# Optimization experiments

Hardware: AMD Instinct MI355X
Metric: run time of the kernel (lower is better)

The kernel has to match this reference:

```python
import jax, jax.numpy as jnp
import numpy as np

EMB = 1024
HEADS = 16
HEAD_DIM = EMB // HEADS
EPS = 1e-5


def setup_inputs() -> dict:
    key = jax.random.key(0)
    ks = jax.random.split(key, 10)
    B, T, D = 2, 2048, EMB
    s = 1.0 / np.sqrt(D)
    inp = {
        "x": jax.random.normal(ks[0], (B, T, D), dtype=jnp.float32),
        "wq": jax.random.normal(ks[1], (D, D), dtype=jnp.float32) * s,
        "bq": jnp.zeros((D,), jnp.float32),
        "wk": jax.random.normal(ks[2], (D, D), dtype=jnp.float32) * s,
        "bk": jnp.zeros((D,), jnp.float32),
        "wv": jax.random.normal(ks[3], (D, D), dtype=jnp.float32) * s,
        "bv": jnp.zeros((D,), jnp.float32),
        "wo": jax.random.normal(ks[4], (D, D), dtype=jnp.float32) * s,
        "bo": jnp.zeros((D,), jnp.float32),
        "gamma": jnp.ones((D,), jnp.float32),
        "beta": jnp.zeros((D,), jnp.float32),
    }
    return inp


def _attention(x, wq, bq, wk, bk, wv, bv, wo, bo, gamma, beta):
    B, T, D = x.shape
    H, Hd = HEADS, HEAD_DIM
    q = (x @ wq + bq).reshape(B, T, H, Hd)
    k = (x @ wk + bk).reshape(B, T, H, Hd)
    v = (x @ wv + bv).reshape(B, T, H, Hd)
    # scores: [B, H, T, T]
    scores = jnp.einsum("bthd,bshd->bhts", q, k) / np.sqrt(Hd)
    attn = jax.nn.softmax(scores, axis=-1)  # dropout is identity in eval
    ctx = jnp.einsum("bhts,bshd->bthd", attn, v).reshape(B, T, D)
    out = ctx @ wo + bo
    y = x + out  # residual (dropout identity)
    mu = jnp.mean(y, axis=-1, keepdims=True)
    var = jnp.var(y, axis=-1, keepdims=True)
    return (y - mu) * jax.lax.rsqrt(var + EPS) * gamma + beta


def reference(x, wq, bq, wk, bk, wv, bv, wo, bo, gamma, beta):
    return _attention(x, wq, bq, wk, bk, wv, bv, wo, bo, gamma, beta)
```

## Files before the change

### kernel.cpp

```cpp
#include <hip/hip_runtime.h>

#define BSZ   2
#define TSEQ  2048
#define DMOD  1024
#define NHEAD 16
#define HDIM  64
#define MROW  (BSZ*TSEQ)
#define LNEPS 1e-5f
#define QSCALE 0.18033688011f

typedef __bf16 bf16x8 __attribute__((ext_vector_type(8)));
typedef float  f32x4  __attribute__((ext_vector_type(4)));
typedef unsigned short us8 __attribute__((ext_vector_type(8)));
typedef unsigned short us4 __attribute__((ext_vector_type(4)));

__device__ __forceinline__ unsigned short f2bf(float f) {
    unsigned u = __float_as_uint(f);
    u += 0x7FFF + ((u >> 16) & 1);
    return (unsigned short)(u >> 16);
}

__device__ __forceinline__ float fexp2(float x) {
#if __has_builtin(__builtin_amdgcn_exp2f)
    return __builtin_amdgcn_exp2f(x);
#else
    return __expf(x * 0.6931471805599453f);
#endif
}

__device__ __forceinline__ void gld_lds16(const void* g, void* l) {
    __builtin_amdgcn_global_load_lds(
        (const __attribute__((address_space(1))) unsigned int*)g,
        (__attribute__((address_space(3))) unsigned int*)l, 16, 0, 0);
}

__global__ __launch_bounds__(256) void cvtx_k(const float* __restrict__ x,
                                              unsigned short* __restrict__ Xb)
{
    const size_t i = ((size_t)blockIdx.x * 256 + threadIdx.x) * 8;
    float4 a = *(const float4*)&x[i];
    float4 b = *(const float4*)&x[i + 4];
    union { unsigned short u[8]; uint4 v; } o;
    o.u[0] = f2bf(a.x); o.u[1] = f2bf(a.y); o.u[2] = f2bf(a.z); o.u[3] = f2bf(a.w);
    o.u[4] = f2bf(b.x); o.u[5] = f2bf(b.y); o.u[6] = f2bf(b.z); o.u[7] = f2bf(b.w);
    *(uint4*)&Xb[i] = o.v;
}

__global__ __launch_bounds__(256) void wt_all_k(
    const float* __restrict__ wq, const float* __restrict__ wk,
    const float* __restrict__ wv, const float* __restrict__ wo,
    unsigned short* __restrict__ WqkvT, unsigned short* __restrict__ WoT)
{
    __shared__ float T[64][68];
    const int z = blockIdx.z;
    const float* W = (z == 0) ? wq : (z == 1) ? wk : (z == 2) ? wv : wo;
    unsigned short* Wt = (z < 3) ? (WqkvT + (size_t)z*1024*1024) : WoT;
    const int tid = threadIdx.x;
    const int bx = blockIdx.x, by = blockIdx.y;
    const int lr = tid >> 4, lc = (tid & 15) * 4;
    #pragma unroll
    for (int p = 0; p < 4; ++p) {
        const int kk = p*16 + lr;
        float4 v = *(const float4*)&W[(size_t)(by*64 + kk)*1024 + bx*64 + lc];
        T[lc+0][kk] = v.x; T[lc+1][kk] = v.y; T[lc+2][kk] = v.z; T[lc+3][kk] = v.w;
    }
    __syncthreads();
    #pragma unroll
    for (int p = 0; p < 2; ++p) {
        const int nl = p*32 + (tid >> 3);
        const int kb = (tid & 7) * 8;
        float4 a = *(const float4*)&T[nl][kb];
        float4 b = *(const float4*)&T[nl][kb+4];
        union { unsigned short u[8]; uint4 v; } o;
        o.u[0]=f2bf(a.x); o.u[1]=f2bf(a.y); o.u[2]=f2bf(a.z); o.u[3]=f2bf(a.w);
        o.u[4]=f2bf(b.x); o.u[5]=f2bf(b.y); o.u[6]=f2bf(b.z); o.u[7]=f2bf(b.w);
        *(uint4*)&Wt[(size_t)(bx*64 + nl)*1024 + by*64 + kb] = o.v;
    }
}

template<int MODE>
__global__ __launch_bounds__(256) void gemm_bf16_k(
    const unsigned short* __restrict__ A, const unsigned short* __restrict__ Bt,
    const float* __restrict__ b0, const float* __restrict__ b1,
    const float* __restrict__ b2,
    void* __restrict__ o0, void* __restrict__ o1, void* __restrict__ o2)
{
    __shared__ unsigned short As[128*32];
    __shared__ unsigned short Bs[128*32];
    const int tid  = threadIdx.x;
    const int wv   = tid >> 6;
    const int lane = tid & 63;
    const int quad = lane >> 4;
    const int l16  = lane & 15;
    const int wm   = wv & 1, wn = wv >> 1;
    const int bm = blockIdx.y * 128, bn = blockIdx.x * 128;

    const int r0 = lane >> 2;
    const int jb = lane & 3;
    const unsigned short* Ag[2]; const unsigned short* Bg[2];
    void *ldsA[2], *ldsB[2];
    #pragma unroll
    for (int j = 0; j < 2; ++j) {
        const int c = wv*2 + j;
        const int R = c*16 + r0;
        const int gb = (jb ^ ((R >> 1) & 3)) * 8;
        Ag[j] = A  + (size_t)(bm + R)*1024 + gb;
        Bg[j] = Bt + (size_t)(bn + R)*1024 + gb;
        ldsA[j] = (char*)As + c*1024;
        ldsB[j] = (char*)Bs + c*1024;
    }

    const int asw = (quad ^ ((l16 >> 1) & 3)) * 8;
    const unsigned short* ap[4]; const unsigned short* bp[4];
    #pragma unroll
    for (int t = 0; t < 4; ++t) {
        ap[t] = &As[(wm*64 + t*16 + l16)*32 + asw];
        bp[t] = &Bs[(wn*64 + t*16 + l16)*32 + asw];
    }

    f32x4 acc[4][4];
    #pragma unroll
    for (int i = 0; i < 4; ++i)
        #pragma unroll
        for (int j = 0; j < 4; ++j) acc[i][j] = (f32x4){0.f,0.f,0.f,0.f};

    for (int k0 = 0; k0 < 1024; k0 += 32) {
        __syncthreads();
        gld_lds16(Ag[0] + k0, ldsA[0]);
        gld_lds16(Ag[1] + k0, ldsA[1]);
        gld_lds16(Bg[0] + k0, ldsB[0]);
        gld_lds16(Bg[1] + k0, ldsB[1]);
        __syncthreads();
        bf16x8 af[4], bfr[4];
        #pragma unroll
        for (int t = 0; t < 4; ++t) {
            af[t]  = *(const bf16x8*)ap[t];
            bfr[t] = *(const bf16x8*)bp[t];
        }
        #pragma unroll
        for (int i = 0; i < 4; ++i)
            #pragma unroll
            for (int j = 0; j < 4; ++j)
                acc[i][j] = __builtin_amdgcn_mfma_f32_16x16x32_bf16(af[i], bfr[j], acc[i][j], 0, 0, 0);
    }

    if (MODE == 0) {
        float* C = (float*)o0;
        #pragma unroll
        for (int nt = 0; nt < 4; ++nt) {
            const int gcol = bn + wn*64 + nt*16 + l16;
            const float bs = b0[gcol];
            #pragma unroll
            for (int mt = 0; mt < 4; ++mt)
                #pragma unroll
                for (int r = 0; r < 4; ++r) {
                    const int grow = bm + wm*64 + mt*16 + quad*4 + r;
                    C[(size_t)grow*1024 + gcol] = acc[mt][nt][r] + bs;
                }
        }
    } else {
        const int seg = bn >> 10;
        const float* bias = (seg == 0) ? b0 : (seg == 1) ? b1 : b2;
        const int cb = bn & 1023;
        if (seg < 2) {
            unsigned short* O = (unsigned short*)((seg == 0) ? o0 : o1);
            const float sc = (seg == 0) ? QSCALE : 1.0f;
            #pragma unroll
            for (int nt = 0; nt < 4; ++nt) {
                const int col = cb + wn*64 + nt*16 + l16;
                const float bs = bias[col];
                #pragma unroll
                for (int mt = 0; mt < 4; ++mt)
                    #pragma unroll
                    for (int r = 0; r < 4; ++r) {
                        const int grow = bm + wm*64 + mt*16 + quad*4 + r;
                        O[(size_t)grow*1024 + col] = f2bf((acc[mt][nt][r] + bs) * sc);
                    }
            }
        } else {
            unsigned short* O = (unsigned short*)o2;
            #pragma unroll
            for (int nt = 0; nt < 4; ++nt) {
                const int ch = cb + wn*64 + nt*16 + l16;
                const float bs = bias[ch];
                #pragma unroll
                for (int mt = 0; mt < 4; ++mt) {
                    const int grow0 = bm + wm*64 + mt*16 + quad*4;
                    us4 o;
                    #pragma unroll
                    for (int r = 0; r < 4; ++r) o[r] = f2bf(acc[mt][nt][r] + bs);
                    *(us4*)&O[(size_t)ch*MROW + grow0] = o;
                }
            }
        }
    }
}

__global__ __launch_bounds__(256, 2) void attn_k(
    const unsigned short* __restrict__ Qg,
    const unsigned short* __restrict__ Kg,
    const unsigned short* __restrict__ Vtg,
    unsigned short* __restrict__ CTX)
{
    __shared__ __align__(16) char lds_raw[51200];
    unsigned short* Qs = (unsigned short*)lds_raw;
    unsigned short* Ks = (unsigned short*)(lds_raw + 18432);
    unsigned short* Vs = (unsigned short*)(lds_raw + 34816);
    float* Od = (float*)lds_raw;
    float* Ld = (float*)(lds_raw + 34816);

    const int tid  = threadIdx.x;
    const int wv   = tid >> 6;
    const int lane = tid & 63;
    const int quad = lane >> 4;
    const int l16  = lane & 15;
    const int wq   = wv & 1;
    const int wk   = wv >> 1;
    const int qb   = blockIdx.x * 128;
    const int h    = blockIdx.y;
    const int b    = blockIdx.z;

    {
        const int row = tid & 127, cb = (tid >> 7) * 32;
        const unsigned short* Qrow = Qg + ((size_t)(b*TSEQ + qb + row))*DMOD + h*HDIM + cb;
        #pragma unroll
        for (int j = 0; j < 4; ++j)
            *(us8*)&Qs[row*72 + cb + j*8] = *(const us8*)&Qrow[j*8];
    }
    __syncthreads();
    bf16x8 qf[4][2];
    #pragma unroll
    for (int nt = 0; nt < 4; ++nt)
        #pragma unroll
        for (int kh = 0; kh < 2; ++kh)
            qf[nt][kh] = *(const bf16x8*)&Qs[(wq*64 + nt*16 + l16)*72 + kh*32 + quad*8];

    const int sr = lane >> 3;
    const int sc = lane & 7;
    const bool isK = (wv < 2);
    const int half = wv & 1;
    const unsigned short* gbase;
    unsigned int goff[8];
    unsigned short* ldst;
    if (isK) {
        gbase = Kg + ((size_t)(b*TSEQ + half*1024))*DMOD + h*HDIM;
        #pragma unroll
        for (int s = 0; s < 8; ++s) {
            const int R = s*8 + sr;
            const int gc = sc ^ ((R ^ (R >> 2)) & 7);
            goff[s] = (unsigned)(R*DMOD + gc*8);
        }
        ldst = Ks + half*4096;
    } else {
        gbase = Vtg + ((size_t)(h*HDIM))*MROW + b*TSEQ + half*1024;
        #pragma unroll
        for (int s = 0; s < 8; ++s) {
            const int D = s*8 + sr;
            const int gc = sc ^ (D & 7);
            goff[s] = (unsigned)(D*MROW + gc*8);
        }
        ldst = Vs + half*4096;
    }
    const size_t gstep = isK ? (size_t)64*DMOD : (size_t)64;

    const int rowA_l = (l16 >> 2)*8 + (l16 & 3);
    const int rowB_l = rowA_l + 4;
    const int swA = (rowA_l ^ (rowA_l >> 2)) & 7;
    const int swB = (rowB_l ^ (rowB_l >> 2)) & 7;
    const unsigned short* KsW = Ks + wk*4096;
    const unsigned short* VsW = Vs + wk*4096;

    bf16x8 onef;
    { union { unsigned short u[8]; bf16x8 v; } o1;
      #pragma unroll
      for (int i = 0; i < 8; ++i) o1.u[i] = 0x3F80;
      onef = o1.v; }

    f32x4 oacc[4][4];
    f32x4 lacc[4];
    #pragma unroll
    for (int dt = 0; dt < 4; ++dt)
        #pragma unroll
        for (int nt = 0; nt < 4; ++nt) oacc[dt][nt] = (f32x4){0.f,0.f,0.f,0.f};
    #pragma unroll
    for (int nt = 0; nt < 4; ++nt) lacc[nt] = (f32x4){0.f,0.f,0.f,0.f};

    for (int it = 0; it < 16; ++it) {
        __syncthreads();
        #pragma unroll
        for (int s = 0; s < 8; ++s)
            gld_lds16(gbase + (size_t)it*gstep + goff[s], ldst + s*512);
        __syncthreads();

        #pragma unroll
        for (int gl = 0; gl < 2; ++gl) {
            const int rA = gl*32 + rowA_l;
            const int rB = gl*32 + rowB_l;
            bf16x8 ka0 = *(const bf16x8*)&KsW[rA*64 + ((quad     ^ swA))*8];
            bf16x8 ka1 = *(const bf16x8*)&KsW[rA*64 + (((4+quad) ^ swA))*8];
            bf16x8 kb0 = *(const bf16x8*)&KsW[rB*64 + ((quad     ^ swB))*8];
            bf16x8 kb1 = *(const bf16x8*)&KsW[rB*64 + (((4+quad) ^ swB))*8];
            bf16x8 vf[4];
            #pragma unroll
            for (int dt = 0; dt < 4; ++dt)
                vf[dt] = *(const bf16x8*)&VsW[(dt*16 + l16)*64 + ((gl*4 + quad) ^ (l16 & 7))*8];

            #pragma unroll
            for (int nt = 0; nt < 4; ++nt) {
                f32x4 z = (f32x4){0.f,0.f,0.f,0.f};
                z = __builtin_amdgcn_mfma_f32_16x16x32_bf16(ka0, qf[nt][0], z, 0, 0, 0);
                f32x4 sA = __builtin_amdgcn_mfma_f32_16x16x32_bf16(ka1, qf[nt][1], z, 0, 0, 0);
                z = (f32x4){0.f,0.f,0.f,0.f};
                z = __builtin_amdgcn_mfma_f32_16x16x32_bf16(kb0, qf[nt][0], z, 0, 0, 0);
                f32x4 sB = __builtin_amdgcn_mfma_f32_16x16x32_bf16(kb1, qf[nt][1], z, 0, 0, 0);

                float eA[4], eB[4];
                #pragma unroll
                for (int r = 0; r < 4; ++r) { eA[r] = fexp2(sA[r]); eB[r] = fexp2(sB[r]); }
                union { unsigned d[4]; bf16x8 v; } up;
                up.d[0] = __builtin_amdgcn_perm(__float_as_uint(eA[1]), __float_as_uint(eA[0]), 0x07060302);
                up.d[1] = __builtin_amdgcn_perm(__float_as_uint(eA[3]), __float_as_uint(eA[2]), 0x07060302);
                up.d[2] = __builtin_amdgcn_perm(__float_as_uint(eB[1]), __float_as_uint(eB[0]), 0x07060302);
                up.d[3] = __builtin_amdgcn_perm(__float_as_uint(eB[3]), __float_as_uint(eB[2]), 0x07060302);
                const bf16x8 pf = up.v;

                lacc[nt] = __builtin_amdgcn_mfma_f32_16x16x32_bf16(onef, pf, lacc[nt], 0, 0, 0);
                #pragma unroll
                for (int dt = 0; dt < 4; ++dt)
                    oacc[dt][nt] = __builtin_amdgcn_mfma_f32_16x16x32_bf16(vf[dt], pf, oacc[dt][nt], 0, 0, 0);
            }
        }
    }

    __syncthreads();
    if (wk == 0) {
        float* od = Od + wq*64*68;
        #pragma unroll
        for (int nt = 0; nt < 4; ++nt) {
            #pragma unroll
            for (int dt = 0; dt < 4; ++dt)
                *(f32x4*)&od[(nt*16 + l16)*68 + dt*16 + quad*4] = oacc[dt][nt];
            if (quad == 0) Ld[wq*64 + nt*16 + l16] = lacc[nt][0];
        }
    }
    __syncthreads();
    if (wk == 1) {
        const float* od = Od + wq*64*68;
        #pragma unroll
        for (int nt = 0; nt < 4; ++nt) {
            const float l = Ld[wq*64 + nt*16 + l16] + lacc[nt][0];
            const float inv = 1.f / l;
            const int q = qb + wq*64 + nt*16 + l16;
            unsigned short* crow = CTX + ((size_t)(b*TSEQ + q))*DMOD + h*HDIM;
            #pragma unroll
            for (int dt = 0; dt < 4; ++dt) {
                f32x4 p = *(const f32x4*)&od[(nt*16 + l16)*68 + dt*16 + quad*4];
                us4 o;
                #pragma unroll
                for (int r = 0; r < 4; ++r) o[r] = f2bf((p[r] + oacc[dt][nt][r]) * inv);
                *(us4*)&crow[dt*16 + quad*4] = o;
            }
        }
    }
}

__global__ __launch_bounds__(256) void ln_k(
    const float* __restrict__ x, float* __restrict__ y,
    const float* __restrict__ gamma, const float* __restrict__ beta)
{
    __shared__ float rs[4], rss[4];
    const int row = blockIdx.x;
    const int tid = threadIdx.x;
    const int c = tid * 4;
    const float4 xv = *(const float4*)&x[(size_t)row*DMOD + c];
    const float4 pv = *(const float4*)&y[(size_t)row*DMOD + c];
    const float v0 = xv.x + pv.x, v1 = xv.y + pv.y;
    const float v2 = xv.z + pv.z, v3 = xv.w + pv.w;
    float s  = v0 + v1 + v2 + v3;
    float ss = v0*v0 + v1*v1 + v2*v2 + v3*v3;
    #pragma unroll
    for (int o = 32; o > 0; o >>= 1) {
        s  += __shfl_down(s,  o, 64);
        ss += __shfl_down(ss, o, 64);
    }
    if ((tid & 63) == 0) { rs[tid >> 6] = s; rss[tid >> 6] = ss; }
    __syncthreads();
    s  = rs[0] + rs[1] + rs[2] + rs[3];
    ss = rss[0] + rss[1] + rss[2] + rss[3];
    const float mean = s * (1.f/DMOD);
    const float var  = ss * (1.f/DMOD) - mean*mean;
    const float rstd = rsqrtf(var + LNEPS);
    const float4 gv = *(const float4*)&gamma[c];
    const float4 bv = *(const float4*)&beta[c];
    float4 o;
    o.x = (v0 - mean)*rstd*gv.x + bv.x;
    o.y = (v1 - mean)*rstd*gv.y + bv.y;
    o.z = (v2 - mean)*rstd*gv.z + bv.z;
    o.w = (v3 - mean)*rstd*gv.w + bv.w;
    *(float4*)&y[(size_t)row*DMOD + c] = o;
}

extern "C" void kernel_launch(void* const* d_in, const int* in_sizes, int n_in,
                              void* d_out, int out_size, void* d_ws, size_t ws_size,
                              hipStream_t stream) {
    const float* x     = (const float*)d_in[0];
    const float* wq    = (const float*)d_in[1];
    const float* bq    = (const float*)d_in[2];
    const float* wk    = (const float*)d_in[3];
    const float* bk    = (const float*)d_in[4];
    const float* wvp   = (const float*)d_in[5];
    const float* bvp   = (const float*)d_in[6];
    const float* wo    = (const float*)d_in[7];
    const float* bo    = (const float*)d_in[8];
    const float* gamma = (const float*)d_in[9];
    const float* beta  = (const float*)d_in[10];
    float* out = (float*)d_out;

    unsigned short* Xb    = (unsigned short*)d_ws;
    unsigned short* WqkvT = Xb    + (size_t)MROW*DMOD;
    unsigned short* WoT   = WqkvT + (size_t)3072*1024;
    unsigned short* Qb    = WoT   + (size_t)1024*1024;
    unsigned short* Kb    = Qb    + (size_t)MROW*DMOD;
    unsigned short* VtG   = Kb    + (size_t)MROW*DMOD;
    unsigned short* CTXb  = VtG   + (size_t)DMOD*MROW;

    cvtx_k<<<(MROW*DMOD)/(256*8), 256, 0, stream>>>(x, Xb);
    wt_all_k<<<dim3(16,16,4), 256, 0, stream>>>(wq, wk, wvp, wo, WqkvT, WoT);

    gemm_bf16_k<1><<<dim3(3072/128, MROW/128), 256, 0, stream>>>(
        Xb, WqkvT, bq, bk, bvp, Qb, Kb, VtG);

    attn_k<<<dim3(TSEQ/128, NHEAD, BSZ), 256, 0, stream>>>(Qb, Kb, VtG, CTXb);

    gemm_bf16_k<0><<<dim3(DMOD/128, MROW/128), 256, 0, stream>>>(
        CTXb, WoT, bo, bo, bo, out, nullptr, nullptr);

    ln_k<<<MROW, 256, 0, stream>>>(x, out, gamma, beta);
}
```

Baseline: 212.3 us.

## Merge prep kernels, deepen GEMM K-tile, split-K output projection with fused reduce+LN

Merges the x conversion and weight transpose kernels into a single launch. The GEMM K step grows from 32 to 64, with a new 8-way XOR swizzle that halves the number of barriers per K. The output projection is split along K into two halves that write bf16 partials into the now-dead Q buffer, which doubles the block count from 256 to 512. The LayerNorm kernel then sums the partials, adds the bias and applies the residual, at the cost of bf16 rounding on the partials and extra partial traffic.

Measured after the change: 195.3 us. -8.0%, faster.

```diff
diff --git a/kernel.cpp b/kernel.cpp
--- a/kernel.cpp
+++ b/kernel.cpp
@@ -19,6 +19,9 @@
     u += 0x7FFF + ((u >> 16) & 1);
     return (unsigned short)(u >> 16);
 }
+__device__ __forceinline__ float bf2f(unsigned short u) {
+    return __uint_as_float((unsigned)u << 16);
+}
 
 __device__ __forceinline__ float fexp2(float x) {
 #if __has_builtin(__builtin_amdgcn_exp2f)
@@ -34,29 +37,31 @@
         (__attribute__((address_space(3))) unsigned int*)l, 16, 0, 0);
 }
 
-__global__ __launch_bounds__(256) void cvtx_k(const float* __restrict__ x,
-                                              unsigned short* __restrict__ Xb)
-{
-    const size_t i = ((size_t)blockIdx.x * 256 + threadIdx.x) * 8;
-    float4 a = *(const float4*)&x[i];
-    float4 b = *(const float4*)&x[i + 4];
-    union { unsigned short u[8]; uint4 v; } o;
-    o.u[0] = f2bf(a.x); o.u[1] = f2bf(a.y); o.u[2] = f2bf(a.z); o.u[3] = f2bf(a.w);
-    o.u[4] = f2bf(b.x); o.u[5] = f2bf(b.y); o.u[6] = f2bf(b.z); o.u[7] = f2bf(b.w);
-    *(uint4*)&Xb[i] = o.v;
-}
-
-__global__ __launch_bounds__(256) void wt_all_k(
+__global__ __launch_bounds__(256) void prep_k(
+    const float* __restrict__ x,
     const float* __restrict__ wq, const float* __restrict__ wk,
     const float* __restrict__ wv, const float* __restrict__ wo,
+    unsigned short* __restrict__ Xb,
     unsigned short* __restrict__ WqkvT, unsigned short* __restrict__ WoT)
 {
+    const int tid = threadIdx.x;
+    if (blockIdx.x < 2048) {
+        const size_t i = ((size_t)blockIdx.x * 256 + tid) * 8;
+        float4 a = *(const float4*)&x[i];
+        float4 b = *(const float4*)&x[i + 4];
+        union { unsigned short u[8]; uint4 v; } o;
+        o.u[0]=f2bf(a.x); o.u[1]=f2bf(a.y); o.u[2]=f2bf(a.z); o.u[3]=f2bf(a.w);
+        o.u[4]=f2bf(b.x); o.u[5]=f2bf(b.y); o.u[6]=f2bf(b.z); o.u[7]=f2bf(b.w);
+        *(uint4*)&Xb[i] = o.v;
+        return;
+    }
     __shared__ float T[64][68];
-    const int z = blockIdx.z;
+    const int id = blockIdx.x - 2048;
+    const int z  = id >> 8;
+    const int bx = id & 15;
+    const int by = (id >> 4) & 15;
     const float* W = (z == 0) ? wq : (z == 1) ? wk : (z == 2) ? wv : wo;
     unsigned short* Wt = (z < 3) ? (WqkvT + (size_t)z*1024*1024) : WoT;
-    const int tid = threadIdx.x;
-    const int bx = blockIdx.x, by = blockIdx.y;
     const int lr = tid >> 4, lc = (tid & 15) * 4;
     #pragma unroll
     for (int p = 0; p < 4; ++p) {
@@ -78,15 +83,83 @@
     }
 }
 
-template<int MODE>
-__global__ __launch_bounds__(256) void gemm_bf16_k(
+struct GemmFrags {
+    const unsigned short* Ag[4]; const unsigned short* Bg[4];
+    unsigned short *la[4], *lb[4];
+    const unsigned short *ap[4][2], *bp[4][2];
+};
+
+__device__ __forceinline__ void gemm_setup(
+    GemmFrags& F, unsigned short* As, unsigned short* Bs,
+    const unsigned short* A, const unsigned short* Bt,
+    int bm, int bn, int lda)
+{
+    const int tid  = threadIdx.x;
+    const int wv   = tid >> 6;
+    const int lane = tid & 63;
+    const int quad = lane >> 4;
+    const int l16  = lane & 15;
+    const int wm   = wv & 1, wn = wv >> 1;
+    const int r_l = lane >> 3;
+    const int c_l = lane & 7;
+    #pragma unroll
+    for (int s = 0; s < 4; ++s) {
+        const int i = wv*4 + s;
+        const int R = i*8 + r_l;
+        const int gc = (c_l ^ (R & 7)) * 8;
+        F.Ag[s] = A  + (size_t)(bm + R)*lda + gc;
+        F.Bg[s] = Bt + (size_t)(bn + R)*lda + gc;
+        F.la[s] = As + i*512;
+        F.lb[s] = Bs + i*512;
+    }
+    #pragma unroll
+    for (int t = 0; t < 4; ++t)
+        #pragma unroll
+        for (int kh = 0; kh < 2; ++kh) {
+            const int ra = wm*64 + t*16 + l16;
+            const int rb = wn*64 + t*16 + l16;
+            F.ap[t][kh] = &As[ra*64 + ((kh*4 + quad) ^ (ra & 7))*8];
+            F.bp[t][kh] = &Bs[rb*64 + ((kh*4 + quad) ^ (rb & 7))*8];
+        }
+}
+
+__device__ __forceinline__ void gemm_kloop(
+    GemmFrags& F, f32x4 (&acc)[4][4], int k_begin, int k_end)
+{
+    for (int k0 = k_begin; k0 < k_end; k0 += 64) {
+        __syncthreads();
+        #pragma unroll
+        for (int s = 0; s < 4; ++s) {
+            gld_lds16(F.Ag[s] + k0, F.la[s]);
+            gld_lds16(F.Bg[s] + k0, F.lb[s]);
+        }
+        __syncthreads();
+        #pragma unroll
+        for (int kh = 0; kh < 2; ++kh) {
+            bf16x8 af[4], bfr[4];
+            #pragma unroll
+            for (int t = 0; t < 4; ++t) {
+                af[t]  = *(const bf16x8*)F.ap[t][kh];
+                bfr[t] = *(const bf16x8*)F.bp[t][kh];
+            }
+            #pragma unroll
+            for (int i = 0; i < 4; ++i)
+                #pragma unroll
+                for (int j = 0; j < 4; ++j)
+                    acc[i][j] = __builtin_amdgcn_mfma_f32_16x16x32_bf16(af[i], bfr[j], acc[i][j], 0, 0, 0);
+        }
+    }
+}
+
+__global__ __launch_bounds__(256) void gemm_qkv_k(
     const unsigned short* __restrict__ A, const unsigned short* __restrict__ Bt,
     const float* __restrict__ b0, const float* __restrict__ b1,
     const float* __restrict__ b2,
-    void* __restrict__ o0, void* __restrict__ o1, void* __restrict__ o2)
-{
-    __shared__ unsigned short As[128*32];
-    __shared__ unsigned short Bs[128*32];
+    unsigned short* __restrict__ oQ, unsigned short* __restrict__ oK,
+    unsigned short* __restrict__ oV)
+{
+    __shared__ unsigned short As[128*64];
+    __shared__ unsigned short Bs[128*64];
     const int tid  = threadIdx.x;
     const int wv   = tid >> 6;
     const int lane = tid & 63;
@@ -95,28 +168,8 @@
     const int wm   = wv & 1, wn = wv >> 1;
     const int bm = blockIdx.y * 128, bn = blockIdx.x * 128;
 
-    const int r0 = lane >> 2;
-    const int jb = lane & 3;
-    const unsigned short* Ag[2]; const unsigned short* Bg[2];
-    void *ldsA[2], *ldsB[2];
-    #pragma unroll
-    for (int j = 0; j < 2; ++j) {
-        const int c = wv*2 + j;
-        const int R = c*16 + r0;
-        const int gb = (jb ^ ((R >> 1) & 3)) * 8;
-        Ag[j] = A  + (size_t)(bm + R)*1024 + gb;
-        Bg[j] = Bt + (size_t)(bn + R)*1024 + gb;
-        ldsA[j] = (char*)As + c*1024;
-        ldsB[j] = (char*)Bs + c*1024;
-    }
-
-    const int asw = (quad ^ ((l16 >> 1) & 3)) * 8;
-    const unsigned short* ap[4]; const unsigned short* bp[4];
-    #pragma unroll
-    for (int t = 0; t < 4; ++t) {
-        ap[t] = &As[(wm*64 + t*16 + l16)*32 + asw];
-        bp[t] = &Bs[(wn*64 + t*16 + l16)*32 + asw];
-    }
+    GemmFrags F;
+    gemm_setup(F, As, Bs, A, Bt, bm, bn, 1024);
 
     f32x4 acc[4][4];
     #pragma unroll
@@ -124,75 +177,80 @@
         #pragma unroll
         for (int j = 0; j < 4; ++j) acc[i][j] = (f32x4){0.f,0.f,0.f,0.f};
 
-    for (int k0 = 0; k0 < 1024; k0 += 32) {
-        __syncthreads();
-        gld_lds16(Ag[0] + k0, ldsA[0]);
-        gld_lds16(Ag[1] + k0, ldsA[1]);
-        gld_lds16(Bg[0] + k0, ldsB[0]);
-        gld_lds16(Bg[1] + k0, ldsB[1]);
-        __syncthreads();
-        bf16x8 af[4], bfr[4];
-        #pragma unroll
-        for (int t = 0; t < 4; ++t) {
-            af[t]  = *(const bf16x8*)ap[t];
-            bfr[t] = *(const bf16x8*)bp[t];
-        }
-        #pragma unroll
-        for (int i = 0; i < 4; ++i)
-            #pragma unroll
-            for (int j = 0; j < 4; ++j)
-                acc[i][j] = __builtin_amdgcn_mfma_f32_16x16x32_bf16(af[i], bfr[j], acc[i][j], 0, 0, 0);
-    }
-
-    if (MODE == 0) {
-        float* C = (float*)o0;
+    gemm_kloop(F, acc, 0, 1024);
+
+    const int seg = bn >> 10;
+    const float* bias = (seg == 0) ? b0 : (seg == 1) ? b1 : b2;
+    const int cb = bn & 1023;
+    if (seg < 2) {
+        unsigned short* O = (seg == 0) ? oQ : oK;
+        const float sc = (seg == 0) ? QSCALE : 1.0f;
         #pragma unroll
         for (int nt = 0; nt < 4; ++nt) {
-            const int gcol = bn + wn*64 + nt*16 + l16;
-            const float bs = b0[gcol];
+            const int col = cb + wn*64 + nt*16 + l16;
+            const float bs = bias[col];
             #pragma unroll
             for (int mt = 0; mt < 4; ++mt)
                 #pragma unroll
                 for (int r = 0; r < 4; ++r) {
                     const int grow = bm + wm*64 + mt*16 + quad*4 + r;
-                    C[(size_t)grow*1024 + gcol] = acc[mt][nt][r] + bs;
+                    O[(size_t)grow*1024 + col] = f2bf((acc[mt][nt][r] + bs) * sc);
                 }
         }
     } else {
-        const int seg = bn >> 10;
-        const float* bias = (seg == 0) ? b0 : (seg == 1) ? b1 : b2;
-        const int cb = bn & 1023;
-        if (seg < 2) {
-            unsigned short* O = (unsigned short*)((seg == 0) ? o0 : o1);
-            const float sc = (seg == 0) ? QSCALE : 1.0f;
-            #pragma unroll
-            for (int nt = 0; nt < 4; ++nt) {
-                const int col = cb + wn*64 + nt*16 + l16;
-                const float bs = bias[col];
+        #pragma unroll
+        for (int nt = 0; nt < 4; ++nt) {
+            const int ch = cb + wn*64 + nt*16 + l16;
+            const float bs = bias[ch];
+            #pragma unroll
+            for (int mt = 0; mt < 4; ++mt) {
+                const int grow0 = bm + wm*64 + mt*16 + quad*4;
+                us4 o;
                 #pragma unroll
-                for (int mt = 0; mt < 4; ++mt)
-                    #pragma unroll
-                    for (int r = 0; r < 4; ++r) {
-                        const int grow = bm + wm*64 + mt*16 + quad*4 + r;
-                        O[(size_t)grow*1024 + col] = f2bf((acc[mt][nt][r] + bs) * sc);
-                    }
+                for (int r = 0; r < 4; ++r) o[r] = f2bf(acc[mt][nt][r] + bs);
+                *(us4*)&oV[(size_t)ch*MROW + grow0] = o;
             }
-        } else {
-            unsigned short* O = (unsigned short*)o2;
-            #pragma unroll
-            for (int nt = 0; nt < 4; ++nt) {
-                const int ch = cb + wn*64 + nt*16 + l16;
-                const float bs = bias[ch];
-                #pragma unroll
-                for (int mt = 0; mt < 4; ++mt) {
-                    const int grow0 = bm + wm*64 + mt*16 + quad*4;
-                    us4 o;
-                    #pragma unroll
-                    for (int r = 0; r < 4; ++r) o[r] = f2bf(acc[mt][nt][r] + bs);
-                    *(us4*)&O[(size_t)ch*MROW + grow0] = o;
-                }
+        }
+    }
+}
+
+__global__ __launch_bounds__(256) void gemm_proj_k(
+    const unsigned short* __restrict__ A, const unsigned short* __restrict__ Bt,
+    unsigned short* __restrict__ P)
+{
+    __shared__ unsigned short As[128*64];
+    __shared__ unsigned short Bs[128*64];
+    const int tid  = threadIdx.x;
+    const int wv   = tid >> 6;
+    const int lane = tid & 63;
+    const int quad = lane >> 4;
+    const int l16  = lane & 15;
+    const int wm   = wv & 1, wn = wv >> 1;
+    const int bm = blockIdx.y * 128, bn = blockIdx.x * 128;
+    const int kz = blockIdx.z;
+
+    GemmFrags F;
+    gemm_setup(F, As, Bs, A, Bt, bm, bn, 1024);
+
+    f32x4 acc[4][4];
+    #pragma unroll
+    for (int i = 0; i < 4; ++i)
+        #pragma unroll
+        for (int j = 0; j < 4; ++j) acc[i][j] = (f32x4){0.f,0.f,0.f,0.f};
+
+    gemm_kloop(F, acc, kz*512, kz*512 + 512);
+
+    unsigned short* O = P + (size_t)kz*MROW*1024;
+    #pragma unroll
+    for (int nt = 0; nt < 4; ++nt) {
+        const int col = bn + wn*64 + nt*16 + l16;
+        #pragma unroll
+        for (int mt = 0; mt < 4; ++mt)
+            #pragma unroll
+            for (int r = 0; r < 4; ++r) {
+                const int grow = bm + wm*64 + mt*16 + quad*4 + r;
+                O[(size_t)grow*1024 + col] = f2bf(acc[mt][nt][r]);
             }
-        }
     }
 }
 
@@ -364,18 +422,24 @@
     }
 }
 
-__global__ __launch_bounds__(256) void ln_k(
-    const float* __restrict__ x, float* __restrict__ y,
-    const float* __restrict__ gamma, const float* __restrict__ beta)
+__global__ __launch_bounds__(256) void red_ln_k(
+    const float* __restrict__ x, const unsigned short* __restrict__ P,
+    const float* __restrict__ bo,
+    const float* __restrict__ gamma, const float* __restrict__ beta,
+    float* __restrict__ out)
 {
     __shared__ float rs[4], rss[4];
     const int row = blockIdx.x;
     const int tid = threadIdx.x;
     const int c = tid * 4;
     const float4 xv = *(const float4*)&x[(size_t)row*DMOD + c];
-    const float4 pv = *(const float4*)&y[(size_t)row*DMOD + c];
-    const float v0 = xv.x + pv.x, v1 = xv.y + pv.y;
-    const float v2 = xv.z + pv.z, v3 = xv.w + pv.w;
+    const us4 p0 = *(const us4*)&P[(size_t)row*DMOD + c];
+    const us4 p1 = *(const us4*)&P[(size_t)(MROW + row)*DMOD + c];
+    const float4 bv4 = *(const float4*)&bo[c];
+    const float v0 = xv.x + bf2f(p0[0]) + bf2f(p1[0]) + bv4.x;
+    const float v1 = xv.y + bf2f(p0[1]) + bf2f(p1[1]) + bv4.y;
+    const float v2 = xv.z + bf2f(p0[2]) + bf2f(p1[2]) + bv4.z;
+    const float v3 = xv.w + bf2f(p0[3]) + bf2f(p1[3]) + bv4.w;
     float s  = v0 + v1 + v2 + v3;
     float ss = v0*v0 + v1*v1 + v2*v2 + v3*v3;
     #pragma unroll
@@ -397,7 +461,7 @@
     o.y = (v1 - mean)*rstd*gv.y + bv.y;
     o.z = (v2 - mean)*rstd*gv.z + bv.z;
     o.w = (v3 - mean)*rstd*gv.w + bv.w;
-    *(float4*)&y[(size_t)row*DMOD + c] = o;
+    *(float4*)&out[(size_t)row*DMOD + c] = o;
 }
 
 extern "C" void kernel_launch(void* const* d_in, const int* in_sizes, int n_in,
@@ -423,17 +487,16 @@
     unsigned short* Kb    = Qb    + (size_t)MROW*DMOD;
     unsigned short* VtG   = Kb    + (size_t)MROW*DMOD;
     unsigned short* CTXb  = VtG   + (size_t)DMOD*MROW;
-
-    cvtx_k<<<(MROW*DMOD)/(256*8), 256, 0, stream>>>(x, Xb);
-    wt_all_k<<<dim3(16,16,4), 256, 0, stream>>>(wq, wk, wvp, wo, WqkvT, WoT);
-
-    gemm_bf16_k<1><<<dim3(3072/128, MROW/128), 256, 0, stream>>>(
+    unsigned short* Pp    = Qb;
+
+    prep_k<<<3072, 256, 0, stream>>>(x, wq, wk, wvp, wo, Xb, WqkvT, WoT);
+
+    gemm_qkv_k<<<dim3(3072/128, MROW/128), 256, 0, stream>>>(
         Xb, WqkvT, bq, bk, bvp, Qb, Kb, VtG);
 
     attn_k<<<dim3(TSEQ/128, NHEAD, BSZ), 256, 0, stream>>>(Qb, Kb, VtG, CTXb);
 
-    gemm_bf16_k<0><<<dim3(DMOD/128, MROW/128), 256, 0, stream>>>(
-        CTXb, WoT, bo, bo, bo, out, nullptr, nullptr);
-
-    ln_k<<<MROW, 256, 0, stream>>>(x, out, gamma, beta);
-}
+    gemm_proj_k<<<dim3(DMOD/128, MROW/128, 2), 256, 0, stream>>>(CTXb, WoT, Pp);
+
+    red_ln_k<<<MROW, 256, 0, stream>>>(x, Pp, bo, gamma, beta, out);
+}
```
